# Performance work log

Hardware: AMD Instinct MI355X
Metric: run time of the kernel (lower is better)

Reference implementation:

```python
import jax, jax.numpy as jnp
import numpy as np

KK = 9   # kH * kW
P = 2    # num_points (len(dilations))


def setup_inputs() -> dict:
    key = jax.random.key(0)
    ks = jax.random.split(key, 12)
    N, A, C, OC = 8000, 4000, 256, 256
    R, rH, rW = 64, 64, 64
    inp = {}
    inp["in_core_feats"] = jax.random.normal(ks[0], (N, C), jnp.float32)
    inp["aux_feats"] = jax.random.normal(ks[1], (A, C), jnp.float32)
    # offset MLP: near-zero weights, bias plays role of the dilation-grid init offsets
    inp["off_w"] = 0.01 * jax.random.normal(ks[2], (KK * P * 2, C), jnp.float32)
    inp["off_b"] = 2.0 * jax.random.uniform(ks[3], (KK * P * 2,), jnp.float32) - 1.0
    inp["pw_w"] = 0.01 * jax.random.normal(ks[4], (KK * P, C), jnp.float32)
    inp["pw_b"] = jnp.zeros((KK * P,), jnp.float32)
    inp["mw_w"] = 0.01 * jax.random.normal(ks[5], (KK, C), jnp.float32)
    inp["mw_b"] = jnp.zeros((KK,), jnp.float32)
    inp["weight"] = jax.random.normal(ks[6], (OC, KK * C), jnp.float32) / np.sqrt(KK * C)
    inp["bias"] = 0.01 * jax.random.normal(ks[7], (OC,), jnp.float32)
    inp["id_map"] = jax.random.randint(ks[8], (R, rH, rW), 0, N + A)
    inp["roi_ids"] = jax.random.randint(ks[9], (N,), 0, R)
    inp["pos_ids"] = jax.random.randint(ks[10], (N, 2), 0, rW)
    return inp


def reference(in_core_feats, aux_feats, off_w, off_b, pw_w, pw_b, mw_w, mw_b,
              weight, bias, id_map, roi_ids, pos_ids):
    N, C = in_core_feats.shape
    # predicted sampling locations in RoI (x, y) coords: [N, KK, P, 2]
    conv_xy = (in_core_feats @ off_w.T + off_b).reshape(N, KK, P, 2)
    conv_xy = pos_ids.astype(conv_xy.dtype)[:, None, None, :] + conv_xy
    floor_xy = jnp.floor(conv_xy)
    base_ids = floor_xy.astype(jnp.int32)
    grid = jnp.array([[0, 0], [1, 0], [0, 1], [1, 1]], jnp.int32)
    cids = base_ids[:, :, :, None, :] + grid            # [N, KK, P, 4, 2]
    cx, cy = cids[..., 0], cids[..., 1]
    rH, rW = id_map.shape[1], id_map.shape[2]
    pad = (cx < 0) | (cy < 0) | (cx >= rW) | (cy >= rH)
    cx = jnp.clip(cx, 0, rW - 1)
    cy = jnp.clip(cy, 0, rH - 1)
    gids = id_map[roi_ids[:, None, None, None], cy, cx]  # [N, KK, P, 4]
    pad_idx = N + aux_feats.shape[0]
    gids = jnp.where(pad, pad_idx, gids)
    # interpolation weights, literal translation of the torch indexing
    delta = conv_xy - floor_xy                           # [N, KK, P, 2]
    dstk = jnp.stack([delta, 1.0 - delta], axis=3)       # [N, KK, P, 2, 2]
    x_ids = jnp.array([1, 0, 1, 0])
    y_ids = jnp.array([1, 1, 0, 0])
    w = dstk[:, :, :, 0, :][..., x_ids] * dstk[:, :, :, 1, :][..., y_ids]  # [N, KK, P, 4]
    # point weights (softmax over points) and modulation weights (sigmoid)
    pw = jax.nn.softmax((in_core_feats @ pw_w.T + pw_b).reshape(N, KK, P), axis=2)
    w = pw[..., None] * w
    mw = jax.nn.sigmoid(in_core_feats @ mw_w.T + mw_b)   # [N, KK]
    w = mw[:, :, None, None] * w
    # gather + weighted reduce over points and corners, then dense matmul
    all_feats = jnp.concatenate(
        [in_core_feats, aux_feats, jnp.zeros((1, C), in_core_feats.dtype)], axis=0)
    sampled = jnp.einsum('nkpgc,nkpg->nkc', all_feats[gids], w)  # [N, KK, C]
    out = sampled.reshape(N, KK * C) @ weight.T + bias
    return out
```

## Files before the change

kernel.cpp:

```cpp
#include <hip/hip_runtime.h>

typedef __attribute__((ext_vector_type(8))) short short8;
typedef __attribute__((ext_vector_type(4))) float f32x4;

static __device__ __forceinline__ unsigned short f2b(float f) {
  union { float f; unsigned int u; } v; v.f = f;
  unsigned int u = v.u;
  unsigned int r = (u + 0x7FFFu + ((u >> 16) & 1u)) >> 16;
  return (unsigned short)r;
}
static __device__ __forceinline__ float b2f(unsigned short u) {
  union { unsigned int u; float f; } v; v.u = ((unsigned int)u) << 16;
  return v.f;
}

__global__ __launch_bounds__(256) void prep_kernel(
    const float* __restrict__ core, const float* __restrict__ aux,
    const float* __restrict__ wgt,
    unsigned short* __restrict__ tab, unsigned short* __restrict__ wB)
{
  const long TAB = 12001L * 256;
  const long WN  = 256L * 2304;
  long i = ((long)blockIdx.x * 256 + threadIdx.x) * 4;
  float4 v;
  unsigned short* dst;
  if (i < TAB) {
    long row = i >> 8;
    if (row < 8000)        v = *(const float4*)(core + i);
    else if (row < 12000)  v = *(const float4*)(aux + (i - 8000L * 256));
    else                   v = make_float4(0.f, 0.f, 0.f, 0.f);
    dst = tab + i;
  } else {
    long j = i - TAB;
    if (j >= WN) return;
    v = *(const float4*)(wgt + j);
    dst = wB + j;
  }
  ushort4 o = make_ushort4(f2b(v.x), f2b(v.y), f2b(v.z), f2b(v.w));
  *(ushort4*)dst = o;
}

__global__ __launch_bounds__(256) void proj_kernel(
    const float* __restrict__ core,
    const float* __restrict__ off_w, const float* __restrict__ off_b,
    const float* __restrict__ pw_w,  const float* __restrict__ pw_b,
    const float* __restrict__ mw_w,  const float* __restrict__ mw_b,
    const int* __restrict__ id_map, const int* __restrict__ roi_ids,
    const int* __restrict__ pos_ids,
    int* __restrict__ gids, float* __restrict__ wts)
{
  __shared__ float dots[32][64];
  const int tid  = threadIdx.x;
  const int lane = tid & 63;
  const int wv   = tid >> 6;
  const int nbase = blockIdx.x * 32 + wv * 8;

  float acc[8] = {0.f,0.f,0.f,0.f,0.f,0.f,0.f,0.f};
  if (lane < 63) {
    const float* wr; float bb;
    if (lane < 36)      { wr = off_w + lane * 256;       bb = off_b[lane]; }
    else if (lane < 54) { wr = pw_w + (lane - 36) * 256; bb = pw_b[lane - 36]; }
    else                { wr = mw_w + (lane - 54) * 256; bb = mw_b[lane - 54]; }
    const float4* w4 = (const float4*)wr;
    #pragma unroll 4
    for (int i = 0; i < 64; ++i) {
      const float4 w = w4[i];
      #pragma unroll
      for (int r = 0; r < 8; ++r) {
        const float4 x = *(const float4*)(core + (long)(nbase + r) * 256 + i * 4);
        acc[r] += w.x * x.x + w.y * x.y + w.z * x.z + w.w * x.w;
      }
    }
    #pragma unroll
    for (int r = 0; r < 8; ++r) acc[r] += bb;
  }
  #pragma unroll
  for (int r = 0; r < 8; ++r) dots[wv * 8 + r][lane] = acc[r];
  __syncthreads();

  #pragma unroll
  for (int round = 0; round < 3; ++round) {
    int task = round * 256 + tid;
    if (task < 576) {
      int nl = task / 18;
      int kp = task - nl * 18;
      int k = kp >> 1, p = kp & 1;
      int n = blockIdx.x * 32 + nl;
      float x = dots[nl][k*4 + p*2 + 0] + (float)pos_ids[n*2 + 0];
      float y = dots[nl][k*4 + p*2 + 1] + (float)pos_ids[n*2 + 1];
      float fx = floorf(x), fy = floorf(y);
      float dx = x - fx, dy = y - fy;
      int bx = (int)fx, by = (int)fy;
      float l0 = dots[nl][36 + k*2], l1 = dots[nl][36 + k*2 + 1];
      float mmax = fmaxf(l0, l1);
      float e0 = __expf(l0 - mmax), e1 = __expf(l1 - mmax);
      float pwv = (p ? e1 : e0) / (e0 + e1);
      float mwv = 1.f / (1.f + __expf(-dots[nl][54 + k]));
      float wb  = pwv * mwv;
      const int* imap = id_map + roi_ids[n] * 4096;
      int base = ((n * 9 + k) * 2 + p) * 4;
      #pragma unroll
      for (int g = 0; g < 4; ++g) {
        int gx = g & 1, gy = g >> 1;
        int cx = bx + gx, cy = by + gy;
        bool pad = ((cx | cy) < 0) | (cx >= 64) | (cy >= 64);
        int cxc = min(max(cx, 0), 63), cyc = min(max(cy, 0), 63);
        int gid = pad ? 12000 : imap[cyc * 64 + cxc];
        float f1 = gx ? dx : dy;
        float f2 = gy ? (1.f - dx) : (1.f - dy);
        gids[base + g] = gid;
        wts[base + g]  = wb * f1 * f2;
      }
    }
  }
}

__global__ __launch_bounds__(256) void gather_kernel(
    const unsigned short* __restrict__ tab,
    const int* __restrict__ gids, const float* __restrict__ wts,
    unsigned short* __restrict__ sampled)
{
  const int lane = threadIdx.x & 63;
  const int wv   = threadIdx.x >> 6;
  const int n    = blockIdx.x * 4 + wv;
  const int c    = lane * 4;
  #pragma unroll
  for (int k = 0; k < 9; ++k) {
    const int jb = (n * 9 + k) * 8;
    float a0 = 0.f, a1 = 0.f, a2 = 0.f, a3 = 0.f;
    #pragma unroll
    for (int j = 0; j < 8; ++j) {
      const int gid = gids[jb + j];
      const float w = wts[jb + j];
      const ushort4 t = *(const ushort4*)(tab + (long)gid * 256 + c);
      a0 += w * b2f(t.x); a1 += w * b2f(t.y);
      a2 += w * b2f(t.z); a3 += w * b2f(t.w);
    }
    ushort4 o = make_ushort4(f2b(a0), f2b(a1), f2b(a2), f2b(a3));
    *(ushort4*)(sampled + ((long)n * 2304 + k * 256 + c)) = o;
  }
}

__global__ __launch_bounds__(256) void gemm_kernel(
    const unsigned short* __restrict__ S,
    const unsigned short* __restrict__ W,
    const float* __restrict__ bias,
    float* __restrict__ out)
{
  __shared__ __align__(16) unsigned short As[64][72];
  __shared__ __align__(16) unsigned short Bs[64][72];
  const int m0 = blockIdx.x * 64;
  const int n0 = blockIdx.y * 64;
  const int t    = threadIdx.x;
  const int lane = t & 63;
  const int wv   = t >> 6;
  const int wr   = wv >> 1, wc = wv & 1;

  f32x4 acc[2][2] = {};

  const int srow = t >> 3;
  const int schk = t & 7;

  for (int kt = 0; kt < 36; ++kt) {
    const int k0 = kt * 64;
    const uint4 ra0 = *(const uint4*)(S + (long)(m0 + srow)      * 2304 + k0 + schk * 8);
    const uint4 ra1 = *(const uint4*)(S + (long)(m0 + srow + 32) * 2304 + k0 + schk * 8);
    const uint4 rb0 = *(const uint4*)(W + (long)(n0 + srow)      * 2304 + k0 + schk * 8);
    const uint4 rb1 = *(const uint4*)(W + (long)(n0 + srow + 32) * 2304 + k0 + schk * 8);
    __syncthreads();
    *(uint4*)&As[srow][schk * 8]      = ra0;
    *(uint4*)&As[srow + 32][schk * 8] = ra1;
    *(uint4*)&Bs[srow][schk * 8]      = rb0;
    *(uint4*)&Bs[srow + 32][schk * 8] = rb1;
    __syncthreads();
    #pragma unroll
    for (int kc = 0; kc < 2; ++kc) {
      const int kk = kc * 32 + (lane >> 4) * 8;
      short8 af[2], bf[2];
      af[0] = *(const short8*)&As[wr * 32 + (lane & 15)][kk];
      af[1] = *(const short8*)&As[wr * 32 + 16 + (lane & 15)][kk];
      bf[0] = *(const short8*)&Bs[wc * 32 + (lane & 15)][kk];
      bf[1] = *(const short8*)&Bs[wc * 32 + 16 + (lane & 15)][kk];
      #pragma unroll
      for (int i = 0; i < 2; ++i)
        #pragma unroll
        for (int j = 0; j < 2; ++j)
          acc[i][j] = __builtin_amdgcn_mfma_f32_16x16x32_bf16(af[i], bf[j], acc[i][j], 0, 0, 0);
    }
  }

  #pragma unroll
  for (int i = 0; i < 2; ++i) {
    const int row = m0 + wr * 32 + i * 16 + (lane >> 4) * 4;
    #pragma unroll
    for (int j = 0; j < 2; ++j) {
      const int col = n0 + wc * 32 + j * 16 + (lane & 15);
      const float bs = bias[col];
      #pragma unroll
      for (int r = 0; r < 4; ++r) {
        out[(long)(row + r) * 256 + col] = acc[i][j][r] + bs;
      }
    }
  }
}

extern "C" void kernel_launch(void* const* d_in, const int* in_sizes, int n_in,
                              void* d_out, int out_size, void* d_ws, size_t ws_size,
                              hipStream_t stream)
{
  const float* core   = (const float*)d_in[0];
  const float* aux    = (const float*)d_in[1];
  const float* off_w  = (const float*)d_in[2];
  const float* off_b  = (const float*)d_in[3];
  const float* pw_w   = (const float*)d_in[4];
  const float* pw_b   = (const float*)d_in[5];
  const float* mw_w   = (const float*)d_in[6];
  const float* mw_b   = (const float*)d_in[7];
  const float* wgt    = (const float*)d_in[8];
  const float* bias   = (const float*)d_in[9];
  const int* id_map   = (const int*)d_in[10];
  const int* roi_ids  = (const int*)d_in[11];
  const int* pos_ids  = (const int*)d_in[12];
  char* ws = (char*)d_ws;

  unsigned short* tab     = (unsigned short*)(ws);
  unsigned short* wB      = (unsigned short*)(ws + 6144512);
  int*            gids    = (int*)           (ws + 7324160);
  float*          wts     = (float*)         (ws + 9628160);
  unsigned short* sampled = (unsigned short*)(ws + 11932160);
  float* out = (float*)d_out;

  hipLaunchKernelGGL(prep_kernel, dim3(3577), dim3(256), 0, stream,
                     core, aux, wgt, tab, wB);
  hipLaunchKernelGGL(proj_kernel, dim3(250), dim3(256), 0, stream,
                     core, off_w, off_b, pw_w, pw_b, mw_w, mw_b,
                     id_map, roi_ids, pos_ids, gids, wts);
  hipLaunchKernelGGL(gather_kernel, dim3(2000), dim3(256), 0, stream,
                     tab, gids, wts, sampled);
  hipLaunchKernelGGL(gemm_kernel, dim3(125, 4), dim3(256), 0, stream,
                     sampled, wB, bias, out);
}
```

Baseline: 176.0 us.

## Merge prep and projection kernels, prefetch gather indices, remap GEMM blocks per XCD

```diff
diff --git a/kernel.cpp b/kernel.cpp
--- a/kernel.cpp
+++ b/kernel.cpp
@@ -14,46 +14,44 @@
   return v.f;
 }
 
-__global__ __launch_bounds__(256) void prep_kernel(
+__global__ __launch_bounds__(256) void setup_kernel(
     const float* __restrict__ core, const float* __restrict__ aux,
     const float* __restrict__ wgt,
-    unsigned short* __restrict__ tab, unsigned short* __restrict__ wB)
-{
-  const long TAB = 12001L * 256;
-  const long WN  = 256L * 2304;
-  long i = ((long)blockIdx.x * 256 + threadIdx.x) * 4;
-  float4 v;
-  unsigned short* dst;
-  if (i < TAB) {
-    long row = i >> 8;
-    if (row < 8000)        v = *(const float4*)(core + i);
-    else if (row < 12000)  v = *(const float4*)(aux + (i - 8000L * 256));
-    else                   v = make_float4(0.f, 0.f, 0.f, 0.f);
-    dst = tab + i;
-  } else {
-    long j = i - TAB;
-    if (j >= WN) return;
-    v = *(const float4*)(wgt + j);
-    dst = wB + j;
-  }
-  ushort4 o = make_ushort4(f2b(v.x), f2b(v.y), f2b(v.z), f2b(v.w));
-  *(ushort4*)dst = o;
-}
-
-__global__ __launch_bounds__(256) void proj_kernel(
-    const float* __restrict__ core,
     const float* __restrict__ off_w, const float* __restrict__ off_b,
     const float* __restrict__ pw_w,  const float* __restrict__ pw_b,
     const float* __restrict__ mw_w,  const float* __restrict__ mw_b,
     const int* __restrict__ id_map, const int* __restrict__ roi_ids,
     const int* __restrict__ pos_ids,
+    unsigned short* __restrict__ tab, unsigned short* __restrict__ wB,
     int* __restrict__ gids, float* __restrict__ wts)
 {
   __shared__ float dots[32][64];
+  if (blockIdx.x < 3577) {
+    const long TAB = 12001L * 256;
+    const long WN  = 256L * 2304;
+    long i = ((long)blockIdx.x * 256 + threadIdx.x) * 4;
+    float4 v;
+    unsigned short* dst;
+    if (i < TAB) {
+      long row = i >> 8;
+      if (row < 8000)        v = *(const float4*)(core + i);
+      else if (row < 12000)  v = *(const float4*)(aux + (i - 8000L * 256));
+      else                   v = make_float4(0.f, 0.f, 0.f, 0.f);
+      dst = tab + i;
+    } else {
+      long j = i - TAB;
+      if (j >= WN) return;
+      v = *(const float4*)(wgt + j);
+      dst = wB + j;
+    }
+    *(ushort4*)dst = make_ushort4(f2b(v.x), f2b(v.y), f2b(v.z), f2b(v.w));
+    return;
+  }
+  const int bid  = blockIdx.x - 3577;
   const int tid  = threadIdx.x;
   const int lane = tid & 63;
   const int wv   = tid >> 6;
-  const int nbase = blockIdx.x * 32 + wv * 8;
+  const int nbase = bid * 32 + wv * 8;
 
   float acc[8] = {0.f,0.f,0.f,0.f,0.f,0.f,0.f,0.f};
   if (lane < 63) {
@@ -85,7 +83,7 @@
       int nl = task / 18;
       int kp = task - nl * 18;
       int k = kp >> 1, p = kp & 1;
-      int n = blockIdx.x * 32 + nl;
+      int n = bid * 32 + nl;
       float x = dots[nl][k*4 + p*2 + 0] + (float)pos_ids[n*2 + 0];
       float y = dots[nl][k*4 + p*2 + 1] + (float)pos_ids[n*2 + 1];
       float fx = floorf(x), fy = floorf(y);
@@ -124,20 +122,38 @@
   const int wv   = threadIdx.x >> 6;
   const int n    = blockIdx.x * 4 + wv;
   const int c    = lane * 4;
+  const long jb  = (long)n * 72;
+
+  int gid[8]; float w[8];
+  #pragma unroll
+  for (int j = 0; j < 8; ++j) { gid[j] = gids[jb + j]; w[j] = wts[jb + j]; }
+
   #pragma unroll
   for (int k = 0; k < 9; ++k) {
-    const int jb = (n * 9 + k) * 8;
+    ushort4 tv[8];
+    #pragma unroll
+    for (int j = 0; j < 8; ++j)
+      tv[j] = *(const ushort4*)(tab + (long)gid[j] * 256 + c);
+    int ngid[8]; float nw[8];
+    if (k < 8) {
+      #pragma unroll
+      for (int j = 0; j < 8; ++j) {
+        ngid[j] = gids[jb + (k + 1) * 8 + j];
+        nw[j]   = wts[jb + (k + 1) * 8 + j];
+      }
+    }
     float a0 = 0.f, a1 = 0.f, a2 = 0.f, a3 = 0.f;
     #pragma unroll
     for (int j = 0; j < 8; ++j) {
-      const int gid = gids[jb + j];
-      const float w = wts[jb + j];
-      const ushort4 t = *(const ushort4*)(tab + (long)gid * 256 + c);
-      a0 += w * b2f(t.x); a1 += w * b2f(t.y);
-      a2 += w * b2f(t.z); a3 += w * b2f(t.w);
-    }
-    ushort4 o = make_ushort4(f2b(a0), f2b(a1), f2b(a2), f2b(a3));
-    *(ushort4*)(sampled + ((long)n * 2304 + k * 256 + c)) = o;
+      a0 += w[j] * b2f(tv[j].x); a1 += w[j] * b2f(tv[j].y);
+      a2 += w[j] * b2f(tv[j].z); a3 += w[j] * b2f(tv[j].w);
+    }
+    *(ushort4*)(sampled + ((long)n * 2304 + k * 256 + c)) =
+        make_ushort4(f2b(a0), f2b(a1), f2b(a2), f2b(a3));
+    if (k < 8) {
+      #pragma unroll
+      for (int j = 0; j < 8; ++j) { gid[j] = ngid[j]; w[j] = nw[j]; }
+    }
   }
 }
 
@@ -149,8 +165,13 @@
 {
   __shared__ __align__(16) unsigned short As[64][72];
   __shared__ __align__(16) unsigned short Bs[64][72];
-  const int m0 = blockIdx.x * 64;
-  const int n0 = blockIdx.y * 64;
+
+  const int orig = blockIdx.x;
+  const int xcd  = orig & 7;
+  const int wgid = (xcd < 4 ? xcd * 63 : 4 * 63 + (xcd - 4) * 62) + (orig >> 3);
+  const int m0 = (wgid >> 2) * 64;
+  const int n0 = (wgid & 3) * 64;
+
   const int t    = threadIdx.x;
   const int lane = t & 63;
   const int wv   = t >> 6;
@@ -197,9 +218,8 @@
       const int col = n0 + wc * 32 + j * 16 + (lane & 15);
       const float bs = bias[col];
       #pragma unroll
-      for (int r = 0; r < 4; ++r) {
+      for (int r = 0; r < 4; ++r)
         out[(long)(row + r) * 256 + col] = acc[i][j][r] + bs;
-      }
     }
   }
 }
@@ -225,18 +245,16 @@
 
   unsigned short* tab     = (unsigned short*)(ws);
   unsigned short* wB      = (unsigned short*)(ws + 6144512);
-  int*            gids    = (int*)           (ws + 7324160);
-  float*          wts     = (float*)         (ws + 9628160);
+  int*            gd      = (int*)           (ws + 7324160);
+  float*          wt      = (float*)         (ws + 9628160);
   unsigned short* sampled = (unsigned short*)(ws + 11932160);
   float* out = (float*)d_out;
 
-  hipLaunchKernelGGL(prep_kernel, dim3(3577), dim3(256), 0, stream,
-                     core, aux, wgt, tab, wB);
-  hipLaunchKernelGGL(proj_kernel, dim3(250), dim3(256), 0, stream,
-                     core, off_w, off_b, pw_w, pw_b, mw_w, mw_b,
-                     id_map, roi_ids, pos_ids, gids, wts);
+  hipLaunchKernelGGL(setup_kernel, dim3(3827), dim3(256), 0, stream,
+                     core, aux, wgt, off_w, off_b, pw_w, pw_b, mw_w, mw_b,
+                     id_map, roi_ids, pos_ids, tab, wB, gd, wt);
   hipLaunchKernelGGL(gather_kernel, dim3(2000), dim3(256), 0, stream,
-                     tab, gids, wts, sampled);
-  hipLaunchKernelGGL(gemm_kernel, dim3(125, 4), dim3(256), 0, stream,
+                     tab, gd, wt, sampled);
+  hipLaunchKernelGGL(gemm_kernel, dim3(500), dim3(256), 0, stream,
                      sampled, wB, bias, out);
 }
```

Measured after the change: 224.5 us. 1.28x slower.
